# Optimization experiments

Measured on AMD Instinct MI355X. Metric: run time of the kernel, lower is better.

Reference implementation:

```python
import jax, jax.numpy as jnp
import numpy as np

EPS = 1e-5
ROPE_BASE = 10000.0

def _rms_norm(x, alpha):
    # var = eps + mean(x^2) (eps added to mean, matching _rms_norm)
    var = EPS + jnp.mean(x * x, axis=-1, keepdims=True)
    return x * (alpha * jax.lax.rsqrt(var))

def _rope(x, pos):
    # x: [B,H,T,D], pos: [T] absolute positions; interleaved pair rotation
    D = x.shape[-1]
    half = D // 2
    inv_freq = ROPE_BASE ** (-jnp.arange(half, dtype=x.dtype) / half)
    ang = pos.astype(x.dtype)[:, None] * inv_freq[None, :]          # [T,half]
    cos, sin = jnp.cos(ang), jnp.sin(ang)
    x1, x2 = x[..., ::2], x[..., 1::2]
    y1 = x1 * cos - x2 * sin
    y2 = x1 * sin + x2 * cos
    return jnp.stack([y1, y2], axis=-1).reshape(x.shape)

def setup_inputs() -> dict:
    key = jax.random.key(0)
    ks = jax.random.split(key, 9)
    B, T, C = 8, 256, 2048
    H, Dh, CAP, FF = 16, 128, 2048, 8192
    s = 0.02
    return {
        "x": jax.random.normal(ks[0], (B, T, C), jnp.float32),
        "kcache": jax.random.normal(ks[1], (B, H, CAP, Dh), jnp.float32) * s,
        "vcache": jax.random.normal(ks[2], (B, H, CAP, Dh), jnp.float32) * s,
        "in_proj_w": jax.random.normal(ks[3], (3 * C, C), jnp.float32) * s,
        "out_proj_w": jax.random.normal(ks[4], (C, C), jnp.float32) * s,
        "norm1_a": jnp.ones((C,), jnp.float32),
        "norm2_a": jnp.ones((C,), jnp.float32),
        "w1": jax.random.normal(ks[5], (FF, C), jnp.float32) * s,
        "w2": jax.random.normal(ks[6], (C, FF), jnp.float32) * s,
        "offset": 1024,
    }

def reference(x, kcache, vcache, in_proj_w, out_proj_w, norm1_a, norm2_a, w1, w2, offset):
    B, T, C = x.shape
    H = 16
    Dh = C // H
    CAP = kcache.shape[2]
    scale = 1.0 / np.sqrt(Dh)

    # ---- self-attention branch ----
    xn = _rms_norm(x, norm1_a)
    qkv = jnp.einsum('btc,oc->bto', xn, in_proj_w)                  # [B,T,3C]
    q, k, v = jnp.split(qkv, 3, axis=-1)
    def heads(t):  # [B,T,C] -> [B,H,T,Dh]
        return t.reshape(B, T, H, Dh).transpose(0, 2, 1, 3)
    q, k, v = heads(q), heads(k), heads(v)

    t_abs = offset + jnp.arange(T)                                   # absolute positions
    q = _rope(q, t_abs)
    k = _rope(k, t_abs)

    # ---- ring KV cache write: idx = (offset + t) % capacity ----
    widx = (offset + jnp.arange(T)) % CAP                            # [T]
    kcache = kcache.at[:, :, widx, :].set(k)
    vcache = vcache.at[:, :, widx, :].set(v)

    # ---- recover absolute positions of cache slots (RingKVCache.complete) ----
    idx = jnp.arange(CAP)
    last = offset + T - 1
    end_index = last % CAP
    delta = idx - end_index
    pos = jnp.where(delta <= 0, last + delta, last + delta - CAP)    # [CAP]
    invalid = idx >= (offset + T)
    pos = jnp.where(invalid, -1, pos)

    # ---- causal + context masked attention over full cache ----
    qpos = offset + jnp.arange(T)                                    # [T]
    d = qpos[:, None] - pos[None, :]                                 # [T,CAP]
    mask = (pos[None, :] >= 0) & (d >= 0) & (d < CAP)
    scores = jnp.einsum('bhtd,bhsd->bhts', q, kcache) * scale        # [B,H,T,CAP]
    scores = jnp.where(mask[None, None], scores, jnp.float32(-1e9))
    attn = jax.nn.softmax(scores, axis=-1)
    o = jnp.einsum('bhts,bhsd->bhtd', attn, vcache)                  # [B,H,T,Dh]
    o = o.transpose(0, 2, 1, 3).reshape(B, T, C)
    x = x + jnp.einsum('btc,oc->bto', o, out_proj_w)

    # ---- MLP branch ----
    h = _rms_norm(x, norm2_a)
    h = jax.nn.gelu(jnp.einsum('btc,fc->btf', h, w1), approximate=False)
    x = x + jnp.einsum('btf,cf->btc', h, w2)
    return x
```

## Files before the change

kernel.cpp:

```cpp
#include <hip/hip_runtime.h>
#include <math.h>


typedef __bf16 bf16_t;
typedef __bf16 bf16x8 __attribute__((ext_vector_type(8)));
typedef float  f32x4  __attribute__((ext_vector_type(4)));

#define MFMA(a, b, c) __builtin_amdgcn_mfma_f32_16x16x32_bf16((a), (b), (c), 0, 0, 0)

static __device__ __forceinline__ bf16x8 cvt8(const float* __restrict__ src) {
    f32x4 f0 = *(const f32x4*)src;
    f32x4 f1 = *(const f32x4*)(src + 4);
    bf16x8 v;
    v[0] = (bf16_t)f0[0]; v[1] = (bf16_t)f0[1]; v[2] = (bf16_t)f0[2]; v[3] = (bf16_t)f0[3];
    v[4] = (bf16_t)f1[0]; v[5] = (bf16_t)f1[1]; v[6] = (bf16_t)f1[2]; v[7] = (bf16_t)f1[3];
    return v;
}

static __device__ __forceinline__ void gload16(const bf16_t* g, bf16_t* lds) {
    __builtin_amdgcn_global_load_lds(
        (const __attribute__((address_space(1))) void*)g,
        (__attribute__((address_space(3))) void*)lds, 16, 0, 0);
}

__global__ __launch_bounds__(256)
void cvt_rows_kernel(const float* __restrict__ src, bf16_t* __restrict__ dst,
                     int cols, int src_stride)
{
    const int row = blockIdx.x;
    const float* s = src + (size_t)row * src_stride;
    bf16_t* d = dst + (size_t)row * cols;
    for (int c = threadIdx.x * 8; c < cols; c += blockDim.x * 8)
        *(bf16x8*)&d[c] = cvt8(&s[c]);
}

__global__ __launch_bounds__(256)
void rmsnorm_kernel(const float* __restrict__ x, const float* __restrict__ alpha,
                    bf16_t* __restrict__ out)
{
    const int C = 2048;
    const int row = blockIdx.x;
    const int tid = threadIdx.x;
    const float* xr = x + (size_t)row * C;
    f32x4 a0 = *(const f32x4*)&xr[tid * 8];
    f32x4 a1 = *(const f32x4*)&xr[tid * 8 + 4];
    float ss = a0[0]*a0[0] + a0[1]*a0[1] + a0[2]*a0[2] + a0[3]*a0[3]
             + a1[0]*a1[0] + a1[1]*a1[1] + a1[2]*a1[2] + a1[3]*a1[3];
    #pragma unroll
    for (int d = 32; d >= 1; d >>= 1) ss += __shfl_xor(ss, d);
    __shared__ float red[4];
    const int lane = tid & 63, wid = tid >> 6;
    if (lane == 0) red[wid] = ss;
    __syncthreads();
    const float tot = red[0] + red[1] + red[2] + red[3];
    const float rs = rsqrtf(1e-5f + tot * (1.0f / C));
    f32x4 l0 = *(const f32x4*)&alpha[tid * 8];
    f32x4 l1 = *(const f32x4*)&alpha[tid * 8 + 4];
    bf16x8 o8;
    o8[0] = (bf16_t)(a0[0] * l0[0] * rs); o8[1] = (bf16_t)(a0[1] * l0[1] * rs);
    o8[2] = (bf16_t)(a0[2] * l0[2] * rs); o8[3] = (bf16_t)(a0[3] * l0[3] * rs);
    o8[4] = (bf16_t)(a1[0] * l1[0] * rs); o8[5] = (bf16_t)(a1[1] * l1[1] * rs);
    o8[6] = (bf16_t)(a1[2] * l1[2] * rs); o8[7] = (bf16_t)(a1[3] * l1[3] * rs);
    *(bf16x8*)&out[(size_t)row * C + tid * 8] = o8;
}

__global__ __launch_bounds__(256)
void reduce_norm_kernel(const bf16_t* __restrict__ p, const float* __restrict__ res,
                        const float* __restrict__ alpha, float* __restrict__ out,
                        bf16_t* __restrict__ hbuf)
{
    const int C = 2048;
    const size_t n = (size_t)2048 * 2048;
    const int row = blockIdx.x;
    const int tid = threadIdx.x;
    const size_t i = (size_t)row * C + tid * 8;
    f32x4 r0 = *(const f32x4*)&res[i];
    f32x4 r1 = *(const f32x4*)&res[i + 4];
    bf16x8 v0 = *(const bf16x8*)&p[i];
    bf16x8 v1 = *(const bf16x8*)&p[n + i];
    r0[0] += (float)v0[0] + (float)v1[0]; r0[1] += (float)v0[1] + (float)v1[1];
    r0[2] += (float)v0[2] + (float)v1[2]; r0[3] += (float)v0[3] + (float)v1[3];
    r1[0] += (float)v0[4] + (float)v1[4]; r1[1] += (float)v0[5] + (float)v1[5];
    r1[2] += (float)v0[6] + (float)v1[6]; r1[3] += (float)v0[7] + (float)v1[7];
    *(f32x4*)&out[i]     = r0;
    *(f32x4*)&out[i + 4] = r1;
    float ss = r0[0]*r0[0] + r0[1]*r0[1] + r0[2]*r0[2] + r0[3]*r0[3]
             + r1[0]*r1[0] + r1[1]*r1[1] + r1[2]*r1[2] + r1[3]*r1[3];
    #pragma unroll
    for (int d = 32; d >= 1; d >>= 1) ss += __shfl_xor(ss, d);
    __shared__ float red[4];
    const int lane = tid & 63, wid = tid >> 6;
    if (lane == 0) red[wid] = ss;
    __syncthreads();
    const float tot = red[0] + red[1] + red[2] + red[3];
    const float rs = rsqrtf(1e-5f + tot * (1.0f / C));
    f32x4 l0 = *(const f32x4*)&alpha[tid * 8];
    f32x4 l1 = *(const f32x4*)&alpha[tid * 8 + 4];
    bf16x8 o8;
    o8[0] = (bf16_t)(r0[0] * l0[0] * rs); o8[1] = (bf16_t)(r0[1] * l0[1] * rs);
    o8[2] = (bf16_t)(r0[2] * l0[2] * rs); o8[3] = (bf16_t)(r0[3] * l0[3] * rs);
    o8[4] = (bf16_t)(r1[0] * l1[0] * rs); o8[5] = (bf16_t)(r1[1] * l1[1] * rs);
    o8[6] = (bf16_t)(r1[2] * l1[2] * rs); o8[7] = (bf16_t)(r1[3] * l1[3] * rs);
    *(bf16x8*)&hbuf[i] = o8;
}

template<int EPI, int NSPLIT>
__global__ __launch_bounds__(256)
void gemm_bb(const bf16_t* __restrict__ A, const bf16_t* __restrict__ B,
             float* Cf, bf16_t* Cb, const float* __restrict__ res,
             int M, int N, int K, int lda, int ldb)
{
    __shared__ bf16_t As[2][128 * 64];
    __shared__ bf16_t Bs[2][128 * 64];
    if constexpr (NSPLIT > 1) {
        A  += (size_t)blockIdx.z * K;
        B  += (size_t)blockIdx.z * K;
        Cb += (size_t)blockIdx.z * (size_t)M * N;
    }
    const int gx = gridDim.x;
    const int orig = blockIdx.y * gx + blockIdx.x;
    const int xcd = orig & 7;
    const int i = orig >> 3;
    const int bw = gx >> 3;
    const int m0 = (i / bw) * 128;
    const int n0 = (xcd * bw + (i % bw)) * 128;

    const int tid = threadIdx.x;
    const int lane = tid & 63, wid = tid >> 6;
    const int wr = wid >> 1, wc = wid & 1;
    const int lr = lane & 15, lg = lane >> 4;
    const int srow = lane >> 3;
    const int scol_swz = (((lane & 7) ^ (lane >> 3)) << 3);
    f32x4 acc[4][4] = {};

    const int nt = K >> 6;
    const bf16_t* Ab = A + (size_t)m0 * lda;
    const bf16_t* Bb = B + (size_t)n0 * ldb;

    #define STAGE(bufi, kt)                                                               \
        _Pragma("unroll")                                                                 \
        for (int it = 0; it < 4; ++it) {                                                  \
            const int r = wid * 32 + it * 8;                                              \
            gload16(&Ab[(size_t)(r + srow) * lda + (kt) + scol_swz], &As[bufi][r * 64]);  \
            gload16(&Bb[(size_t)(r + srow) * ldb + (kt) + scol_swz], &Bs[bufi][r * 64]);  \
        }

    STAGE(0, 0);
    __syncthreads();
    int cur = 0;
    for (int t = 0; t < nt; ++t) {
        if (t + 1 < nt) STAGE(cur ^ 1, (t + 1) << 6);
        __builtin_amdgcn_s_setprio(1);
        #pragma unroll
        for (int kk = 0; kk < 2; ++kk) {
            bf16x8 af[4], bfr[4];
            #pragma unroll
            for (int m = 0; m < 4; ++m)
                af[m] = *(const bf16x8*)&As[cur][(wr * 64 + m * 16 + lr) * 64
                                                 + (((kk * 4 + lg) ^ (lr & 7)) << 3)];
            #pragma unroll
            for (int n = 0; n < 4; ++n)
                bfr[n] = *(const bf16x8*)&Bs[cur][(wc * 64 + n * 16 + lr) * 64
                                                  + (((kk * 4 + lg) ^ (lr & 7)) << 3)];
            #pragma unroll
            for (int m = 0; m < 4; ++m)
                #pragma unroll
                for (int n = 0; n < 4; ++n)
                    acc[m][n] = MFMA(af[m], bfr[n], acc[m][n]);
        }
        __builtin_amdgcn_s_setprio(0);
        __syncthreads();
        cur ^= 1;
    }
    #undef STAGE

    #pragma unroll
    for (int m = 0; m < 4; ++m) {
        #pragma unroll
        for (int n = 0; n < 4; ++n) {
            const int gmb = m0 + wr * 64 + m * 16 + lg * 4;
            const int gn  = n0 + wc * 64 + n * 16 + lr;
            #pragma unroll
            for (int r = 0; r < 4; ++r) {
                const size_t off = (size_t)(gmb + r) * N + gn;
                const float v = acc[m][n][r];
                if (EPI == 0)      Cf[off] = v;
                else if (EPI == 1) Cf[off] = res[off] + v;
                else if (EPI == 2) Cb[off] = (bf16_t)(0.5f * v * (1.0f + erff(v * 0.70710678118654752f)));
                else               Cb[off] = (bf16_t)v;
            }
        }
    }
}

template<int Z>
__global__ __launch_bounds__(256)
void reduce_sk_kernel(const bf16_t* __restrict__ p, const float* __restrict__ res,
                      float* __restrict__ out, int n)
{
    for (int i = (blockIdx.x * 256 + threadIdx.x) * 8; i < n; i += gridDim.x * 256 * 8) {
        f32x4 r0 = *(const f32x4*)&res[i];
        f32x4 r1 = *(const f32x4*)&res[i + 4];
        #pragma unroll
        for (int z = 0; z < Z; ++z) {
            bf16x8 v = *(const bf16x8*)&p[(size_t)z * n + i];
            r0[0] += (float)v[0]; r0[1] += (float)v[1]; r0[2] += (float)v[2]; r0[3] += (float)v[3];
            r1[0] += (float)v[4]; r1[1] += (float)v[5]; r1[2] += (float)v[6]; r1[3] += (float)v[7];
        }
        *(f32x4*)&out[i] = r0;
        *(f32x4*)&out[i + 4] = r1;
    }
}

__global__ __launch_bounds__(256)
void rope_split_kernel(const bf16_t* __restrict__ qkv,
                       bf16_t* __restrict__ q, bf16_t* __restrict__ kn,
                       bf16_t* __restrict__ vn, const int* __restrict__ offp)
{
    const int m = blockIdx.x;
    const int b = m >> 8, t = m & 255;
    const int tid = threadIdx.x;
    const int c = tid * 8;
    const int h = c >> 7, d0 = c & 127;
    const int pos = offp[0] + t;
    bf16x8 qv = *(const bf16x8*)&qkv[(size_t)m * 6144 + c];
    bf16x8 kv = *(const bf16x8*)&qkv[(size_t)m * 6144 + 2048 + c];
    bf16x8 vv = *(const bf16x8*)&qkv[(size_t)m * 6144 + 4096 + c];
    bf16x8 qo, ko;
    #pragma unroll
    for (int p = 0; p < 4; ++p) {
        const int i = (d0 >> 1) + p;
        const float ang = (float)pos * __expf(-(float)i * 0.14391156861538527f);
        const float sn = sinf(ang), cs = cosf(ang);
        const float q1 = (float)qv[2 * p], q2 = (float)qv[2 * p + 1];
        const float k1 = (float)kv[2 * p], k2 = (float)kv[2 * p + 1];
        qo[2 * p]     = (bf16_t)(q1 * cs - q2 * sn);
        qo[2 * p + 1] = (bf16_t)(q1 * sn + q2 * cs);
        ko[2 * p]     = (bf16_t)(k1 * cs - k2 * sn);
        ko[2 * p + 1] = (bf16_t)(k1 * sn + k2 * cs);
    }
    const size_t oi = (((size_t)(b * 16 + h) * 256) + t) * 128 + d0;
    *(bf16x8*)&q[oi]  = qo;
    *(bf16x8*)&kn[oi] = ko;
    *(bf16x8*)&vn[oi] = vv;
}

__global__ __launch_bounds__(256)
void attn_kernel(const bf16_t* __restrict__ qh, const bf16_t* __restrict__ kn,
                 const bf16_t* __restrict__ vn, const float* __restrict__ kcache,
                 const float* __restrict__ vcache, bf16_t* __restrict__ outp,
                 const int* __restrict__ offp)
{
    const int T = 256, Dh = 128, CAP = 2048, H = 16;
    const float scale = 0.08838834764831845f;
    __shared__ bf16_t Ks[64][136];
    __shared__ bf16_t VtL[128 * 64];
    __shared__ bf16_t Pl[4][16][72];
    const int bh = blockIdx.x;
    const int t0 = blockIdx.y * 64;
    const int b = bh >> 4, h = bh & 15;
    const int offset = offp[0];
    const int Stot = offset + T;
    const int tid = threadIdx.x, lane = tid & 63, wid = tid >> 6;
    const int lr = lane & 15, lg = lane >> 4;

    bf16x8 qf[4];
    {
        const bf16_t* qbase = qh + ((size_t)bh * T + t0 + wid * 16) * Dh;
        #pragma unroll
        for (int ks = 0; ks < 4; ++ks)
            qf[ks] = *(const bf16x8*)&qbase[lr * Dh + ks * 32 + lg * 8];
    }
    f32x4 accO[8] = {};
    float mrun[4], lrun[4];
    #pragma unroll
    for (int r = 0; r < 4; ++r) { mrun[r] = -3e38f; lrun[r] = 0.0f; }

    int smax = offset + t0 + 64; if (smax > Stot) smax = Stot;
    const int nch = (smax + 63) >> 6;

    for (int ch = 0; ch < nch; ++ch) {
        const int s0 = ch * 64;
        __syncthreads();
        #pragma unroll
        for (int it = 0; it < 4; ++it) {
            const int idx = tid + it * 256;
            const int r = idx >> 4, c8 = idx & 15;
            const int s = s0 + r;
            bf16x8 kv8, vv8;
            if (s < offset) {
                const size_t base = (((size_t)b * H + h) * CAP + s) * Dh + c8 * 8;
                kv8 = cvt8(&kcache[base]);
                vv8 = cvt8(&vcache[base]);
            } else if (s < Stot) {
                const size_t base = ((size_t)bh * T + (s - offset)) * Dh + c8 * 8;
                kv8 = *(const bf16x8*)&kn[base];
                vv8 = *(const bf16x8*)&vn[base];
            } else {
                #pragma unroll
                for (int j = 0; j < 8; ++j) { kv8[j] = (bf16_t)0.0f; vv8[j] = (bf16_t)0.0f; }
            }
            *(bf16x8*)&Ks[r][c8 * 8] = kv8;
            #pragma unroll
            for (int j = 0; j < 8; ++j)
                VtL[(c8 * 8 + j) * 64 + ((((r >> 3) ^ j ^ (c8 & 7))) << 3) + (r & 7)] = vv8[j];
        }
        __syncthreads();

        f32x4 sc[4] = {};
        #pragma unroll
        for (int ks = 0; ks < 4; ++ks) {
            bf16x8 kf[4];
            #pragma unroll
            for (int n = 0; n < 4; ++n)
                kf[n] = *(const bf16x8*)&Ks[n * 16 + lr][ks * 32 + lg * 8];
            #pragma unroll
            for (int n = 0; n < 4; ++n)
                sc[n] = MFMA(qf[ks], kf[n], sc[n]);
        }

        #pragma unroll
        for (int r = 0; r < 4; ++r) {
            const int qpos = offset + t0 + wid * 16 + lg * 4 + r;
            float mx = -3e38f;
            #pragma unroll
            for (int n = 0; n < 4; ++n) {
                const int sabs = s0 + n * 16 + lr;
                float v = sc[n][r] * scale;
                v = (sabs <= qpos && sabs < Stot) ? v : -1e30f;
                sc[n][r] = v;
                mx = fmaxf(mx, v);
            }
            #pragma unroll
            for (int d = 8; d >= 1; d >>= 1) mx = fmaxf(mx, __shfl_xor(mx, d));
            const float mo = mrun[r];
            const float mn2 = fmaxf(mo, mx);
            const float al = __expf(mo - mn2);
            mrun[r] = mn2;
            lrun[r] *= al;
            #pragma unroll
            for (int df = 0; df < 8; ++df) accO[df][r] *= al;
            float rsum = 0.0f;
            #pragma unroll
            for (int n = 0; n < 4; ++n) {
                const float p = __expf(sc[n][r] - mn2);
                sc[n][r] = p;
                rsum += p;
            }
            #pragma unroll
            for (int d = 8; d >= 1; d >>= 1) rsum += __shfl_xor(rsum, d);
            lrun[r] += rsum;
            #pragma unroll
            for (int n = 0; n < 4; ++n)
                Pl[wid][lg * 4 + r][n * 16 + lr] = (bf16_t)sc[n][r];
        }
        asm volatile("s_waitcnt lgkmcnt(0)" ::: "memory");
        __builtin_amdgcn_sched_barrier(0);

        #pragma unroll
        for (int ks2 = 0; ks2 < 2; ++ks2) {
            const bf16x8 pa = *(const bf16x8*)&Pl[wid][lr][ks2 * 32 + lg * 8];
            #pragma unroll
            for (int df = 0; df < 8; ++df) {
                const int d = df * 16 + lr;
                const bf16x8 vb8 = *(const bf16x8*)
                    &VtL[d * 64 + (((ks2 * 4 + lg) ^ (d & 7) ^ ((d >> 3) & 7)) << 3)];
                accO[df] = MFMA(pa, vb8, accO[df]);
            }
        }
    }

    float rinv[4];
    #pragma unroll
    for (int r = 0; r < 4; ++r) rinv[r] = 1.0f / lrun[r];
    #pragma unroll
    for (int df = 0; df < 8; ++df) {
        #pragma unroll
        for (int r = 0; r < 4; ++r) {
            const int t = t0 + wid * 16 + lg * 4 + r;
            outp[((size_t)b * 256 + t) * 2048 + h * 128 + df * 16 + lr] =
                (bf16_t)(accO[df][r] * rinv[r]);
        }
    }
}

extern "C" void kernel_launch(void* const* d_in, const int* in_sizes, int n_in,
                              void* d_out, int out_size, void* d_ws, size_t ws_size,
                              hipStream_t stream)
{
    const float* x    = (const float*)d_in[0];
    const float* kc   = (const float*)d_in[1];
    const float* vc   = (const float*)d_in[2];
    const float* wqkv = (const float*)d_in[3];
    const float* wo   = (const float*)d_in[4];
    const float* a1   = (const float*)d_in[5];
    const float* a2   = (const float*)d_in[6];
    const float* w1   = (const float*)d_in[7];
    const float* w2   = (const float*)d_in[8];
    const int*   offp = (const int*)d_in[9];
    float* out = (float*)d_out;

    char* ws = (char*)d_ws;
    bf16_t* xn     = (bf16_t*)(ws + 0);
    bf16_t* wqkv_b = (bf16_t*)(ws + (8ull  << 20));
    bf16_t* qkv    = (bf16_t*)(ws + (32ull << 20));
    bf16_t* q      = (bf16_t*)(ws + (8ull  << 20));
    bf16_t* kn     = (bf16_t*)(ws + (16ull << 20));
    bf16_t* vn     = (bf16_t*)(ws + (24ull << 20));
    bf16_t* wo_b   = (bf16_t*)(ws + (32ull << 20));
    bf16_t* o      = (bf16_t*)(ws + (40ull << 20));
    bf16_t* oprt   = (bf16_t*)(ws + (48ull << 20));
    bf16_t* hbuf   = (bf16_t*)(ws + 0);
    const bool bigws = ws_size >= (137ull << 20);

    rmsnorm_kernel<<<2048, 256, 0, stream>>>(x, a1, xn);
    cvt_rows_kernel<<<6144, 256, 0, stream>>>(wqkv, wqkv_b, 2048, 2048);
    gemm_bb<3, 1><<<dim3(48, 16), 256, 0, stream>>>(xn, wqkv_b, nullptr, qkv, nullptr,
                                                    2048, 6144, 2048, 2048, 2048);
    rope_split_kernel<<<2048, 256, 0, stream>>>(qkv, q, kn, vn, offp);
    cvt_rows_kernel<<<2048, 256, 0, stream>>>(wo, wo_b, 2048, 2048);
    attn_kernel<<<dim3(128, 4), 256, 0, stream>>>(q, kn, vn, kc, vc, o, offp);
    gemm_bb<3, 2><<<dim3(16, 16, 2), 256, 0, stream>>>(o, wo_b, nullptr, oprt, nullptr,
                                                       2048, 2048, 1024, 2048, 2048);
    reduce_norm_kernel<<<2048, 256, 0, stream>>>(oprt, x, a2, out, hbuf);

    if (bigws) {
        bf16_t* w1b = (bf16_t*)(ws + (8ull   << 20));
        bf16_t* g   = (bf16_t*)(ws + (40ull  << 20));
        bf16_t* w2b = (bf16_t*)(ws + (72ull  << 20));
        bf16_t* prt = (bf16_t*)(ws + (104ull << 20));
        cvt_rows_kernel<<<8192, 256, 0, stream>>>(w1, w1b, 2048, 2048);
        gemm_bb<2, 1><<<dim3(64, 16), 256, 0, stream>>>(hbuf, w1b, nullptr, g, nullptr,
                                                        2048, 8192, 2048, 2048, 2048);
        cvt_rows_kernel<<<2048, 256, 0, stream>>>(w2, w2b, 8192, 8192);
        gemm_bb<3, 4><<<dim3(16, 16, 4), 256, 0, stream>>>(g, w2b, nullptr, prt, nullptr,
                                                           2048, 2048, 2048, 8192, 8192);
        reduce_sk_kernel<4><<<2048, 256, 0, stream>>>(prt, out, out, 2048 * 2048);
    } else {
        bf16_t* w1b = (bf16_t*)(ws + (8ull  << 20));
        bf16_t* g_h = (bf16_t*)(ws + (24ull << 20));
        bf16_t* w2b = (bf16_t*)(ws + (40ull << 20));
        bf16_t* prt = (bf16_t*)(ws + (8ull  << 20));
        for (int hh = 0; hh < 2; ++hh) {
            cvt_rows_kernel<<<4096, 256, 0, stream>>>(w1 + (size_t)hh * 4096 * 2048, w1b, 2048, 2048);
            gemm_bb<2, 1><<<dim3(32, 16), 256, 0, stream>>>(hbuf, w1b, nullptr, g_h, nullptr,
                                                            2048, 4096, 2048, 2048, 2048);
            cvt_rows_kernel<<<2048, 256, 0, stream>>>(w2 + (size_t)hh * 4096, w2b, 4096, 8192);
            gemm_bb<3, 2><<<dim3(16, 16, 2), 256, 0, stream>>>(g_h, w2b, nullptr, prt, nullptr,
                                                               2048, 2048, 2048, 4096, 4096);
            reduce_sk_kernel<2><<<2048, 256, 0, stream>>>(prt, out, out, 2048 * 2048);
        }
    }
}
```

Baseline: 447.0 us.

## Pre-convert KV cache to bf16 with transposed V and double-buffered async attention

When workspace is large, a new prep kernel converts the valid prefix of the fp32 K/V cache to bf16 once, merges it with the freshly computed K/V, and stores V transposed. A new attention kernel then streams these bf16 tiles into double-buffered LDS with async global-to-LDS loads and XOR swizzling, overlapping the next tile's load with the current tile's compute. The aim is to take fp32 conversion and transposition out of the attention inner loop. The cost is an extra kernel launch and additional global traffic to write and re-read the bf16 buffers. The smaller-workspace path keeps the old kernel.

```diff
diff --git a/kernel.cpp b/kernel.cpp
--- a/kernel.cpp
+++ b/kernel.cpp
@@ -214,8 +214,9 @@
 
 __global__ __launch_bounds__(256)
 void rope_split_kernel(const bf16_t* __restrict__ qkv,
-                       bf16_t* __restrict__ q, bf16_t* __restrict__ kn,
-                       bf16_t* __restrict__ vn, const int* __restrict__ offp)
+                       bf16_t* __restrict__ q, bf16_t* __restrict__ kout,
+                       bf16_t* __restrict__ vn, const int* __restrict__ offp,
+                       int S, int useoff)
 {
     const int m = blockIdx.x;
     const int b = m >> 8, t = m & 255;
@@ -223,6 +224,7 @@
     const int c = tid * 8;
     const int h = c >> 7, d0 = c & 127;
     const int pos = offp[0] + t;
+    const int soff = useoff ? offp[0] : 0;
     bf16x8 qv = *(const bf16x8*)&qkv[(size_t)m * 6144 + c];
     bf16x8 kv = *(const bf16x8*)&qkv[(size_t)m * 6144 + 2048 + c];
     bf16x8 vv = *(const bf16x8*)&qkv[(size_t)m * 6144 + 4096 + c];
@@ -239,17 +241,199 @@
         ko[2 * p]     = (bf16_t)(k1 * cs - k2 * sn);
         ko[2 * p + 1] = (bf16_t)(k1 * sn + k2 * cs);
     }
-    const size_t oi = (((size_t)(b * 16 + h) * 256) + t) * 128 + d0;
-    *(bf16x8*)&q[oi]  = qo;
-    *(bf16x8*)&kn[oi] = ko;
-    *(bf16x8*)&vn[oi] = vv;
-}
-
-__global__ __launch_bounds__(256)
-void attn_kernel(const bf16_t* __restrict__ qh, const bf16_t* __restrict__ kn,
-                 const bf16_t* __restrict__ vn, const float* __restrict__ kcache,
-                 const float* __restrict__ vcache, bf16_t* __restrict__ outp,
-                 const int* __restrict__ offp)
+    const int bh = b * 16 + h;
+    *(bf16x8*)&q[(((size_t)bh * 256) + t) * 128 + d0]        = qo;
+    *(bf16x8*)&kout[(((size_t)bh * S) + soff + t) * 128 + d0] = ko;
+    *(bf16x8*)&vn[(((size_t)bh * 256) + t) * 128 + d0]       = vv;
+}
+
+__global__ __launch_bounds__(256)
+void kv_prep_kernel(const float* __restrict__ kc, const float* __restrict__ vc,
+                    const bf16_t* __restrict__ vn, bf16_t* __restrict__ Kall,
+                    bf16_t* __restrict__ Vtall, const int* __restrict__ offp)
+{
+    const int CAP = 2048;
+    const int bh = blockIdx.x;
+    const int s0 = blockIdx.y * 64;
+    const int offset = offp[0];
+    const int tid = threadIdx.x;
+    __shared__ bf16_t Vt_lds[64][136];
+    if (s0 < offset) {
+        #pragma unroll
+        for (int it = 0; it < 4; ++it) {
+            const int idx = tid + it * 256;
+            const int r = idx >> 4, c8 = idx & 15;
+            const size_t base = ((size_t)bh * CAP + s0 + r) * 128 + c8 * 8;
+            *(bf16x8*)&Kall[((size_t)bh * 1280 + s0 + r) * 128 + c8 * 8] = cvt8(&kc[base]);
+            *(bf16x8*)&Vt_lds[r][c8 * 8] = cvt8(&vc[base]);
+        }
+    } else {
+        #pragma unroll
+        for (int it = 0; it < 4; ++it) {
+            const int idx = tid + it * 256;
+            const int r = idx >> 4, c8 = idx & 15;
+            *(bf16x8*)&Vt_lds[r][c8 * 8] =
+                *(const bf16x8*)&vn[((size_t)bh * 256 + (s0 - offset) + r) * 128 + c8 * 8];
+        }
+    }
+    __syncthreads();
+    const int d = tid >> 1, sh = (tid & 1) * 32;
+    #pragma unroll
+    for (int g = 0; g < 4; ++g) {
+        bf16x8 o;
+        #pragma unroll
+        for (int j = 0; j < 8; ++j) o[j] = Vt_lds[sh + g * 8 + j][d];
+        *(bf16x8*)&Vtall[((size_t)bh * 128 + d) * 1280 + s0 + sh + g * 8] = o;
+    }
+}
+
+__global__ __launch_bounds__(256)
+void attn_pf_kernel(const bf16_t* __restrict__ qh, const bf16_t* __restrict__ Kall,
+                    const bf16_t* __restrict__ Vtall, bf16_t* __restrict__ outp,
+                    const int* __restrict__ offp)
+{
+    const float scale = 0.08838834764831845f;
+    __shared__ bf16_t Ks[2][64 * 128];
+    __shared__ bf16_t VtL[2][128 * 64];
+    __shared__ bf16_t Pl[4][16][72];
+    const int bh = blockIdx.x;
+    const int t0 = blockIdx.y * 64;
+    const int b = bh >> 4, h = bh & 15;
+    const int offset = offp[0];
+    const int Stot = offset + 256;
+    const int tid = threadIdx.x, lane = tid & 63, wid = tid >> 6;
+    const int lr = lane & 15, lg = lane >> 4;
+
+    bf16x8 qf[4];
+    {
+        const bf16_t* qbase = qh + ((size_t)bh * 256 + t0 + wid * 16) * 128;
+        #pragma unroll
+        for (int ks = 0; ks < 4; ++ks)
+            qf[ks] = *(const bf16x8*)&qbase[lr * 128 + ks * 32 + lg * 8];
+    }
+    f32x4 accO[8] = {};
+    float mrun[4], lrun[4];
+    #pragma unroll
+    for (int r = 0; r < 4; ++r) { mrun[r] = -3e38f; lrun[r] = 0.0f; }
+
+    int smax = offset + t0 + 64; if (smax > Stot) smax = Stot;
+    const int nch = (smax + 63) >> 6;
+
+    const bf16_t* Kb = Kall + (size_t)bh * 1280 * 128;
+    const bf16_t* Vb = Vtall + (size_t)bh * 128 * 1280;
+
+    #define ASTAGE(bufi, ss)                                                              \
+        _Pragma("unroll")                                                                 \
+        for (int it = 0; it < 4; ++it) {                                                  \
+            const int br = (wid * 4 + it) * 4;                                            \
+            gload16(&Kb[((size_t)(ss) + br + (lane >> 4)) * 128                           \
+                        + (((lane & 15) ^ ((br + (lane >> 4)) & 15)) << 3)],              \
+                    &Ks[bufi][br * 128]);                                                 \
+            const int bd = (wid * 4 + it) * 8;                                            \
+            gload16(&Vb[(size_t)(bd + (lane >> 3)) * 1280 + (ss)                          \
+                        + (((lane & 7) ^ ((bd + (lane >> 3)) & 7)) << 3)],                \
+                    &VtL[bufi][bd * 64]);                                                 \
+        }
+
+    ASTAGE(0, 0);
+    __syncthreads();
+    int cur = 0;
+    for (int ch = 0; ch < nch; ++ch) {
+        const int s0 = ch * 64;
+        if (ch + 1 < nch) ASTAGE(cur ^ 1, s0 + 64);
+
+        __builtin_amdgcn_s_setprio(1);
+        f32x4 sc[4] = {};
+        #pragma unroll
+        for (int ks = 0; ks < 4; ++ks) {
+            bf16x8 kf[4];
+            #pragma unroll
+            for (int n = 0; n < 4; ++n) {
+                const int row = n * 16 + lr;
+                kf[n] = *(const bf16x8*)&Ks[cur][row * 128
+                                                 + (((ks * 4 + lg) ^ (row & 15)) << 3)];
+            }
+            #pragma unroll
+            for (int n = 0; n < 4; ++n)
+                sc[n] = MFMA(qf[ks], kf[n], sc[n]);
+        }
+        __builtin_amdgcn_s_setprio(0);
+
+        #pragma unroll
+        for (int r = 0; r < 4; ++r) {
+            const int qpos = offset + t0 + wid * 16 + lg * 4 + r;
+            float mx = -3e38f;
+            #pragma unroll
+            for (int n = 0; n < 4; ++n) {
+                const int sabs = s0 + n * 16 + lr;
+                float v = sc[n][r] * scale;
+                v = (sabs <= qpos && sabs < Stot) ? v : -1e30f;
+                sc[n][r] = v;
+                mx = fmaxf(mx, v);
+            }
+            #pragma unroll
+            for (int d = 8; d >= 1; d >>= 1) mx = fmaxf(mx, __shfl_xor(mx, d));
+            const float mo = mrun[r];
+            const float mn2 = fmaxf(mo, mx);
+            const float al = __expf(mo - mn2);
+            mrun[r] = mn2;
+            lrun[r] *= al;
+            #pragma unroll
+            for (int df = 0; df < 8; ++df) accO[df][r] *= al;
+            float rsum = 0.0f;
+            #pragma unroll
+            for (int n = 0; n < 4; ++n) {
+                const float p = __expf(sc[n][r] - mn2);
+                sc[n][r] = p;
+                rsum += p;
+            }
+            #pragma unroll
+            for (int d = 8; d >= 1; d >>= 1) rsum += __shfl_xor(rsum, d);
+            lrun[r] += rsum;
+            #pragma unroll
+            for (int n = 0; n < 4; ++n)
+                Pl[wid][lg * 4 + r][n * 16 + lr] = (bf16_t)sc[n][r];
+        }
+        asm volatile("s_waitcnt lgkmcnt(0)" ::: "memory");
+        __builtin_amdgcn_sched_barrier(0);
+
+        __builtin_amdgcn_s_setprio(1);
+        #pragma unroll
+        for (int ks2 = 0; ks2 < 2; ++ks2) {
+            const bf16x8 pa = *(const bf16x8*)&Pl[wid][lr][ks2 * 32 + lg * 8];
+            #pragma unroll
+            for (int df = 0; df < 8; ++df) {
+                const int d = df * 16 + lr;
+                const bf16x8 vb8 = *(const bf16x8*)&VtL[cur][d * 64
+                                        + (((ks2 * 4 + lg) ^ (d & 7)) << 3)];
+                accO[df] = MFMA(pa, vb8, accO[df]);
+            }
+        }
+        __builtin_amdgcn_s_setprio(0);
+        __syncthreads();
+        cur ^= 1;
+    }
+    #undef ASTAGE
+
+    float rinv[4];
+    #pragma unroll
+    for (int r = 0; r < 4; ++r) rinv[r] = 1.0f / lrun[r];
+    #pragma unroll
+    for (int df = 0; df < 8; ++df) {
+        #pragma unroll
+        for (int r = 0; r < 4; ++r) {
+            const int t = t0 + wid * 16 + lg * 4 + r;
+            outp[((size_t)b * 256 + t) * 2048 + h * 128 + df * 16 + lr] =
+                (bf16_t)(accO[df][r] * rinv[r]);
+        }
+    }
+}
+
+__global__ __launch_bounds__(256)
+void attn_sb_kernel(const bf16_t* __restrict__ qh, const bf16_t* __restrict__ kn,
+                    const bf16_t* __restrict__ vn, const float* __restrict__ kcache,
+                    const float* __restrict__ vcache, bf16_t* __restrict__ outp,
+                    const int* __restrict__ offp)
 {
     const int T = 256, Dh = 128, CAP = 2048, H = 16;
     const float scale = 0.08838834764831845f;
@@ -401,34 +585,37 @@
     float* out = (float*)d_out;
 
     char* ws = (char*)d_ws;
-    bf16_t* xn     = (bf16_t*)(ws + 0);
-    bf16_t* wqkv_b = (bf16_t*)(ws + (8ull  << 20));
-    bf16_t* qkv    = (bf16_t*)(ws + (32ull << 20));
-    bf16_t* q      = (bf16_t*)(ws + (8ull  << 20));
-    bf16_t* kn     = (bf16_t*)(ws + (16ull << 20));
-    bf16_t* vn     = (bf16_t*)(ws + (24ull << 20));
-    bf16_t* wo_b   = (bf16_t*)(ws + (32ull << 20));
-    bf16_t* o      = (bf16_t*)(ws + (40ull << 20));
-    bf16_t* oprt   = (bf16_t*)(ws + (48ull << 20));
-    bf16_t* hbuf   = (bf16_t*)(ws + 0);
     const bool bigws = ws_size >= (137ull << 20);
 
-    rmsnorm_kernel<<<2048, 256, 0, stream>>>(x, a1, xn);
-    cvt_rows_kernel<<<6144, 256, 0, stream>>>(wqkv, wqkv_b, 2048, 2048);
-    gemm_bb<3, 1><<<dim3(48, 16), 256, 0, stream>>>(xn, wqkv_b, nullptr, qkv, nullptr,
-                                                    2048, 6144, 2048, 2048, 2048);
-    rope_split_kernel<<<2048, 256, 0, stream>>>(qkv, q, kn, vn, offp);
-    cvt_rows_kernel<<<2048, 256, 0, stream>>>(wo, wo_b, 2048, 2048);
-    attn_kernel<<<dim3(128, 4), 256, 0, stream>>>(q, kn, vn, kc, vc, o, offp);
-    gemm_bb<3, 2><<<dim3(16, 16, 2), 256, 0, stream>>>(o, wo_b, nullptr, oprt, nullptr,
-                                                       2048, 2048, 1024, 2048, 2048);
-    reduce_norm_kernel<<<2048, 256, 0, stream>>>(oprt, x, a2, out, hbuf);
-
     if (bigws) {
-        bf16_t* w1b = (bf16_t*)(ws + (8ull   << 20));
-        bf16_t* g   = (bf16_t*)(ws + (40ull  << 20));
-        bf16_t* w2b = (bf16_t*)(ws + (72ull  << 20));
-        bf16_t* prt = (bf16_t*)(ws + (104ull << 20));
+        bf16_t* xn     = (bf16_t*)(ws + 0);
+        bf16_t* wqkv_b = (bf16_t*)(ws + (8ull   << 20));
+        bf16_t* qkv    = (bf16_t*)(ws + (96ull  << 20));
+        bf16_t* q      = (bf16_t*)(ws + 0);
+        bf16_t* vn_t   = (bf16_t*)(ws + (8ull   << 20));
+        bf16_t* Kall   = (bf16_t*)(ws + (16ull  << 20));
+        bf16_t* Vtall  = (bf16_t*)(ws + (56ull  << 20));
+        bf16_t* wo_b   = (bf16_t*)(ws + (96ull  << 20));
+        bf16_t* o      = (bf16_t*)(ws + (104ull << 20));
+        bf16_t* oprt   = (bf16_t*)(ws + (112ull << 20));
+        bf16_t* hbuf   = (bf16_t*)(ws + 0);
+        bf16_t* w1b    = (bf16_t*)(ws + (8ull   << 20));
+        bf16_t* g      = (bf16_t*)(ws + (40ull  << 20));
+        bf16_t* w2b    = (bf16_t*)(ws + (72ull  << 20));
+        bf16_t* prt    = (bf16_t*)(ws + (104ull << 20));
+
+        rmsnorm_kernel<<<2048, 256, 0, stream>>>(x, a1, xn);
+        cvt_rows_kernel<<<6144, 256, 0, stream>>>(wqkv, wqkv_b, 2048, 2048);
+        gemm_bb<3, 1><<<dim3(48, 16), 256, 0, stream>>>(xn, wqkv_b, nullptr, qkv, nullptr,
+                                                        2048, 6144, 2048, 2048, 2048);
+        rope_split_kernel<<<2048, 256, 0, stream>>>(qkv, q, Kall, vn_t, offp, 1280, 1);
+        kv_prep_kernel<<<dim3(128, 20), 256, 0, stream>>>(kc, vc, vn_t, Kall, Vtall, offp);
+        cvt_rows_kernel<<<2048, 256, 0, stream>>>(wo, wo_b, 2048, 2048);
+        attn_pf_kernel<<<dim3(128, 4), 256, 0, stream>>>(q, Kall, Vtall, o, offp);
+        gemm_bb<3, 2><<<dim3(16, 16, 2), 256, 0, stream>>>(o, wo_b, nullptr, oprt, nullptr,
+                                                           2048, 2048, 1024, 2048, 2048);
+        reduce_norm_kernel<<<2048, 256, 0, stream>>>(oprt, x, a2, out, hbuf);
+
         cvt_rows_kernel<<<8192, 256, 0, stream>>>(w1, w1b, 2048, 2048);
         gemm_bb<2, 1><<<dim3(64, 16), 256, 0, stream>>>(hbuf, w1b, nullptr, g, nullptr,
                                                         2048, 8192, 2048, 2048, 2048);
@@ -437,6 +624,28 @@
                                                            2048, 2048, 2048, 8192, 8192);
         reduce_sk_kernel<4><<<2048, 256, 0, stream>>>(prt, out, out, 2048 * 2048);
     } else {
+        bf16_t* xn     = (bf16_t*)(ws + 0);
+        bf16_t* wqkv_b = (bf16_t*)(ws + (8ull  << 20));
+        bf16_t* qkv    = (bf16_t*)(ws + (32ull << 20));
+        bf16_t* q      = (bf16_t*)(ws + (8ull  << 20));
+        bf16_t* kn     = (bf16_t*)(ws + (16ull << 20));
+        bf16_t* vn     = (bf16_t*)(ws + (24ull << 20));
+        bf16_t* wo_b   = (bf16_t*)(ws + (32ull << 20));
+        bf16_t* o      = (bf16_t*)(ws + (40ull << 20));
+        bf16_t* oprt   = (bf16_t*)(ws + (48ull << 20));
+        bf16_t* hbuf   = (bf16_t*)(ws + 0);
+
+        rmsnorm_kernel<<<2048, 256, 0, stream>>>(x, a1, xn);
+        cvt_rows_kernel<<<6144, 256, 0, stream>>>(wqkv, wqkv_b, 2048, 2048);
+        gemm_bb<3, 1><<<dim3(48, 16), 256, 0, stream>>>(xn, wqkv_b, nullptr, qkv, nullptr,
+                                                        2048, 6144, 2048, 2048, 2048);
+        rope_split_kernel<<<2048, 256, 0, stream>>>(qkv, q, kn, vn, offp, 256, 0);
+        cvt_rows_kernel<<<2048, 256, 0, stream>>>(wo, wo_b, 2048, 2048);
+        attn_sb_kernel<<<dim3(128, 4), 256, 0, stream>>>(q, kn, vn, kc, vc, o, offp);
+        gemm_bb<3, 2><<<dim3(16, 16, 2), 256, 0, stream>>>(o, wo_b, nullptr, oprt, nullptr,
+                                                           2048, 2048, 1024, 2048, 2048);
+        reduce_norm_kernel<<<2048, 256, 0, stream>>>(oprt, x, a2, out, hbuf);
+
         bf16_t* w1b = (bf16_t*)(ws + (8ull  << 20));
         bf16_t* g_h = (bf16_t*)(ws + (24ull << 20));
         bf16_t* w2b = (bf16_t*)(ws + (40ull << 20));
```

Result: no change. 449.4 us (+0.5%).
